# Optimization experiments

Measured on AMD Instinct MI355X. Metric: run time of the kernel, lower is better.

The kernel has to match this reference:

```python
import jax, jax.numpy as jnp
import numpy as np

M, N, K, D_IN = 200, 6, 25, 784
GAMMA, EPS = 0.5, 0.5
TOTAL = M * N


def setup_inputs() -> dict:
    key = jax.random.key(0)
    ks = jax.random.split(key, 8)
    B = 16384
    def lin(kk, shape, fan_in):
        bound = 1.0 / np.sqrt(fan_in)
        return jax.random.uniform(kk, shape, jnp.float32, -bound, bound)
    return {
        "batch_x": jax.random.normal(ks[0], (B, D_IN), jnp.float32),
        "Wa": lin(ks[1], (M, D_IN), D_IN),
        "ba": lin(ks[2], (M,), D_IN),
        "Wb": lin(ks[3], (TOTAL, TOTAL), TOTAL),
        "bb": lin(ks[4], (TOTAL,), TOTAL),
        "Wd": lin(ks[5], (D_IN, M), M),
        "bd": lin(ks[6], (D_IN,), M),
    }


def _step(params, carry, x):
    Wa, ba, Wb, bb, Wd, bd = params
    x_b, phi, psi = carry
    # sigma: per-group drive broadcast over cells + full recurrent term, shape (m, n)
    z_a = (Wa @ x + ba)[:, None]                      # (m, 1)
    z_b = (Wb @ x_b + bb).reshape(M, N)               # (m, n)
    sigma = z_a + z_b
    # inhibited activity
    pi = (1.0 - phi) * (sigma - sigma.min() + 1.0)    # (m, n)
    lambda_i = pi.max(axis=1)                         # (m,)
    # top-1 cell per group (scatter of topk indices == one-hot argmax)
    M_pi = jax.nn.one_hot(jnp.argmax(pi, axis=1), N, dtype=sigma.dtype)
    # top-k groups
    _, idx = jax.lax.top_k(lambda_i, K)
    M_lambda = jnp.zeros((M,), sigma.dtype).at[idx].set(1.0)[:, None]
    y = jnp.tanh(M_pi * M_lambda * sigma)             # (m, n)
    x_a_pred = Wd @ y.max(axis=1) + bd                # (D_in,)
    # memory / inhibition updates
    psi_n = jnp.maximum(EPS * psi, y)
    phi_n = jnp.maximum(GAMMA * phi, y)
    alpha = psi_n.sum()
    alpha = jnp.where(alpha == 0.0, 1.0, alpha)
    x_b_n = (psi_n / alpha).reshape(-1)
    # original detaches the recurrent state each step
    carry_n = (jax.lax.stop_gradient(x_b_n),
               jax.lax.stop_gradient(phi_n),
               jax.lax.stop_gradient(psi_n))
    return carry_n, x_a_pred


def reference(batch_x, Wa, ba, Wb, bb, Wd, bd):
    params = (Wa, ba, Wb, bb, Wd, bd)
    carry0 = (jnp.zeros((TOTAL,), batch_x.dtype),
              jnp.zeros((M, N), batch_x.dtype),
              jnp.zeros((M, N), batch_x.dtype))
    (x_b, phi, psi), preds = jax.lax.scan(
        lambda c, x: _step(params, c, x), carry0, batch_x)
    return preds, x_b, phi, psi
```

## Files before the change

kernel.cpp:

```cpp
#include <hip/hip_runtime.h>
#include <math.h>

#define Tn   16384
#define Mg   200
#define Nc   6
#define TOT  1200
#define Kk   25
#define Din  784
#define CH   32

__global__ void transpose_k(const float* __restrict__ src, float* __restrict__ dst,
                            int R, int C) {
    __shared__ float tile[32][33];
    int bx = blockIdx.x * 32, by = blockIdx.y * 32;
    int x = bx + threadIdx.x;
    for (int j = 0; j < 32; j += 8) {
        int y = by + threadIdx.y + j;
        if (x < C && y < R) tile[threadIdx.y + j][threadIdx.x] = src[(size_t)y * C + x];
    }
    __syncthreads();
    int x2 = by + threadIdx.x;
    for (int j = 0; j < 32; j += 8) {
        int y2 = bx + threadIdx.y + j;
        if (x2 < R && y2 < C) dst[(size_t)y2 * R + x2] = tile[threadIdx.x][threadIdx.y + j];
    }
}

__global__ void za_k(const float* __restrict__ X, const float* __restrict__ Wa,
                     const float* __restrict__ ba, float* __restrict__ Za) {
    __shared__ float xs[16][788];
    const int tid = threadIdx.x;
    const int t0  = blockIdx.x * 16;
    for (int idx = tid; idx < 16 * Din; idx += 256) {
        int tt = idx / Din, kk = idx - tt * Din;
        xs[tt][kk] = X[(size_t)(t0 + tt) * Din + kk];
    }
    __syncthreads();
    const int tq = tid & 15, gq = tid >> 4;
    const float4* xrow = reinterpret_cast<const float4*>(&xs[tq][0]);
    for (int g = gq; g < Mg; g += 16) {
        float acc = ba[g];
        const float4* wrow = reinterpret_cast<const float4*>(Wa + (size_t)g * Din);
        for (int k4 = 0; k4 < Din / 4; ++k4) {
            float4 a = xrow[k4], b = wrow[k4];
            acc = fmaf(a.x, b.x, acc); acc = fmaf(a.y, b.y, acc);
            acc = fmaf(a.z, b.z, acc); acc = fmaf(a.w, b.w, acc);
        }
        Za[(size_t)(t0 + tq) * Mg + g] = acc;
    }
}

__launch_bounds__(256, 1)
__global__ void serial_k(const float* __restrict__ Za, const float* __restrict__ WbT,
                         const float* __restrict__ bb,
                         unsigned long long* __restrict__ YP,
                         float* __restrict__ outTail) {
    __shared__ alignas(16) unsigned long long lamk[Mg];
    __shared__ alignas(16) unsigned long long sel[26];
    __shared__ alignas(16) float red[4];
    __shared__ alignas(16) float zs[CH * Mg];
    __shared__ alignas(16) unsigned long long ypk[CH * Kk];

    const int tid = threadIdx.x;
    const bool own = (tid < Mg);
    const int b = Nc * tid;

    float u0=0.f,u1=0.f,u2=0.f,u3=0.f,u4=0.f,u5=0.f;
    float p0=0.f,p1=0.f,p2=0.f,p3=0.f,p4=0.f,p5=0.f;
    float b0=0.f,b1=0.f,b2=0.f,b3=0.f,b4=0.f,b5=0.f;
    float alpha = 0.f;
    if (own) {
        b0=bb[b]; b1=bb[b+1]; b2=bb[b+2]; b3=bb[b+3]; b4=bb[b+4]; b5=bb[b+5];
    }
    #pragma unroll
    for (int i = 0; i < 7; ++i) {
        int idx = i * 1024 + tid * 4;
        if (idx < CH * Mg) {
            float4 v = *reinterpret_cast<const float4*>(Za + idx);
            *reinterpret_cast<float4*>(zs + idx) = v;
        }
    }
    __syncthreads();

    const float* baseW = WbT + b;

    for (int t = 0; t < Tn; ++t) {
        const int tc = t & (CH - 1);

        float s0=0,s1=0,s2=0,s3=0,s4=0,s5=0;
        float lmin = INFINITY;
        if (own) {
            float zbv = zs[tc * Mg + tid];
            float inv = (alpha == 0.f) ? 1.f : (1.f / alpha);
            s0 = fmaf(u0, inv, b0 + zbv); s1 = fmaf(u1, inv, b1 + zbv);
            s2 = fmaf(u2, inv, b2 + zbv); s3 = fmaf(u3, inv, b3 + zbv);
            s4 = fmaf(u4, inv, b4 + zbv); s5 = fmaf(u5, inv, b5 + zbv);
            lmin = fminf(fminf(fminf(s0,s1),fminf(s2,s3)),fminf(s4,s5));
        }
        for (int o = 32; o; o >>= 1) lmin = fminf(lmin, __shfl_down(lmin, o));
        if ((tid & 63) == 0) red[tid >> 6] = lmin;
        __syncthreads();

        unsigned long long myk = 0ull;
        float sb=0.f, pb=0.f; int bj = 0;
        if (own) {
            float4 r4 = *reinterpret_cast<const float4*>(red);
            float m1 = 1.f - fminf(fminf(r4.x, r4.y), fminf(r4.z, r4.w));
            float best = -INFINITY;
            float sa[6] = {s0,s1,s2,s3,s4,s5};
            float pa[6] = {p0,p1,p2,p3,p4,p5};
            #pragma unroll
            for (int j = 0; j < Nc; ++j) {
                float pv = (1.f - pa[j]) * (sa[j] + m1);
                if (pv > best) { best = pv; bj = j; sb = sa[j]; pb = pa[j]; }
            }
            unsigned ub = __float_as_uint(best);
            ub ^= (unsigned)(((int)ub) >> 31) | 0x80000000u;
            myk = ((unsigned long long)ub << 32) | (unsigned long long)(0xFFFFFFFFu - (unsigned)tid);
            lamk[tid] = myk;
        }
        __syncthreads();

        if (own) {
            float y  = tanhf(sb);
            float yv = fmaxf(y, 0.f);
            float dc = fmaxf(y - 0.5f * pb, 0.f);
            int r = 0;
            const ulonglong2* L = reinterpret_cast<const ulonglong2*>(lamk);
            #pragma unroll
            for (int qq = 0; qq < Mg / 2; ++qq) {
                ulonglong2 kv = L[qq];
                r += (kv.x > myk) + (kv.y > myk);
            }
            float d = 0.f;
            if (r < Kk) {
                d = dc;
                sel[r] = ((unsigned long long)(unsigned)((b + bj) * TOT) << 32) |
                         (unsigned long long)__float_as_uint(d);
                ypk[tc * Kk + r] = ((unsigned long long)(unsigned)tid << 32) |
                                   (unsigned long long)__float_as_uint(yv);
            }
            p0 = 0.5f*p0 + ((bj==0)?d:0.f); p1 = 0.5f*p1 + ((bj==1)?d:0.f);
            p2 = 0.5f*p2 + ((bj==2)?d:0.f); p3 = 0.5f*p3 + ((bj==3)?d:0.f);
            p4 = 0.5f*p4 + ((bj==4)?d:0.f); p5 = 0.5f*p5 + ((bj==5)?d:0.f);
        }
        __syncthreads();

        if (own) {
            ulonglong2 sraw[13];
            const ulonglong2* S = reinterpret_cast<const ulonglong2*>(sel);
            #pragma unroll
            for (int qq = 0; qq < 13; ++qq) sraw[qq] = S[qq];
            float sd[Kk]; int so[Kk];
            #pragma unroll
            for (int k = 0; k < Kk; ++k) {
                unsigned long long v = (k & 1) ? sraw[k >> 1].y : sraw[k >> 1].x;
                sd[k] = __uint_as_float((unsigned)v);
                so[k] = (int)(v >> 32);
            }
            float asum = 0.f;
            #pragma unroll
            for (int k = 0; k < Kk; ++k) asum += sd[k];
            alpha = 0.5f * alpha + asum;

            float2 c0[Kk], c1[Kk], c2[Kk];
            #pragma unroll
            for (int k = 0; k < Kk; ++k) {
                const float* cp = baseW + so[k];
                c0[k] = *reinterpret_cast<const float2*>(cp);
                c1[k] = *reinterpret_cast<const float2*>(cp + 2);
                c2[k] = *reinterpret_cast<const float2*>(cp + 4);
            }
            __builtin_amdgcn_sched_barrier(0);
            float a0=0.5f*u0, a1=0.5f*u1, a2=0.5f*u2, a3=0.5f*u3, a4=0.5f*u4, a5=0.5f*u5;
            #pragma unroll
            for (int k = 0; k < Kk; ++k) {
                float dk = sd[k];
                a0 = fmaf(dk, c0[k].x, a0); a1 = fmaf(dk, c0[k].y, a1);
                a2 = fmaf(dk, c1[k].x, a2); a3 = fmaf(dk, c1[k].y, a3);
                a4 = fmaf(dk, c2[k].x, a4); a5 = fmaf(dk, c2[k].y, a5);
            }
            u0=a0; u1=a1; u2=a2; u3=a3; u4=a4; u5=a5;
        }

        if (tc == CH - 1) {
            const size_t t0 = (size_t)(t - (CH - 1)) * Kk;
            for (int i = tid; i < CH * Kk; i += 256)
                YP[t0 + i] = ypk[i];
            if (t + 1 < Tn) {
                const float* src = Za + (size_t)(t + 1) * Mg;
                #pragma unroll
                for (int i = 0; i < 7; ++i) {
                    int idx = i * 1024 + tid * 4;
                    if (idx < CH * Mg) {
                        float4 v = *reinterpret_cast<const float4*>(src + idx);
                        *reinterpret_cast<float4*>(zs + idx) = v;
                    }
                }
            }
            __syncthreads();
        }
    }

    if (own) {
        float inv = (alpha == 0.f) ? 1.f : (1.f / alpha);
        float pa[6] = {p0,p1,p2,p3,p4,p5};
        #pragma unroll
        for (int j = 0; j < Nc; ++j) {
            outTail[b + j]           = pa[j] * inv;
            outTail[TOT + b + j]     = pa[j];
            outTail[2 * TOT + b + j] = pa[j];
        }
    }
}

__global__ void preds_k(const unsigned long long* __restrict__ YP,
                        const float* __restrict__ WdT, const float* __restrict__ bd,
                        float* __restrict__ out) {
    const int t = blockIdx.x;
    __shared__ float sv[Kk];
    __shared__ int   si[Kk];
    if (threadIdx.x < Kk) {
        unsigned long long v = YP[(size_t)t * Kk + threadIdx.x];
        sv[threadIdx.x] = __uint_as_float((unsigned)v);
        si[threadIdx.x] = (int)(v >> 32);
    }
    __syncthreads();
    for (int d = threadIdx.x; d < Din; d += 256) {
        float acc = bd[d];
        #pragma unroll
        for (int k = 0; k < Kk; ++k)
            acc = fmaf(sv[k], WdT[(size_t)si[k] * Din + d], acc);
        out[(size_t)t * Din + d] = acc;
    }
}

extern "C" void kernel_launch(void* const* d_in, const int* in_sizes, int n_in,
                              void* d_out, int out_size, void* d_ws, size_t ws_size,
                              hipStream_t stream) {
    const float* X  = (const float*)d_in[0];
    const float* Wa = (const float*)d_in[1];
    const float* ba = (const float*)d_in[2];
    const float* Wb = (const float*)d_in[3];
    const float* bb = (const float*)d_in[4];
    const float* Wd = (const float*)d_in[5];
    const float* bd = (const float*)d_in[6];
    float* out = (float*)d_out;

    float* w    = (float*)d_ws;
    float* Za   = w;
    float* WbT  = Za  + (size_t)Tn * Mg;
    float* WdT  = WbT + (size_t)TOT * TOT;
    unsigned long long* YP =
        (unsigned long long*)(WdT + (size_t)Mg * Din);

    dim3 tb(32, 8);
    transpose_k<<<dim3((TOT + 31) / 32, (TOT + 31) / 32), tb, 0, stream>>>(Wb, WbT, TOT, TOT);
    transpose_k<<<dim3((Mg + 31) / 32, (Din + 31) / 32), tb, 0, stream>>>(Wd, WdT, Din, Mg);
    za_k<<<Tn / 16, 256, 0, stream>>>(X, Wa, ba, Za);
    serial_k<<<1, 256, 0, stream>>>(Za, WbT, bb, YP, out + (size_t)Tn * Din);
    preds_k<<<Tn, 256, 0, stream>>>(YP, WdT, bd, out);
}
```

Baseline: 78.09 ms.

## Run serial recurrence in a single wavefront with ballot-based top-k selection

The serial kernel shrinks from 256 threads to a single 64-lane wavefront, with each lane owning four groups (24 cells). Block-wide __syncthreads barriers and the O(M) rank-counting top-k are replaced by wave shuffles for the min and a ballot/popcount quickselect for the 25th-largest key. It also swaps tanhf for an exp/rcp approximation and double-buffers the float4 weight-row loads. In exchange, each lane does four times the per-step work and holds much more register state, and the quickselect loop has a data-dependent iteration count.

```diff
diff --git a/kernel.cpp b/kernel.cpp
--- a/kernel.cpp
+++ b/kernel.cpp
@@ -50,166 +50,235 @@
     }
 }
 
-__launch_bounds__(256, 1)
+__launch_bounds__(64, 1)
 __global__ void serial_k(const float* __restrict__ Za, const float* __restrict__ WbT,
                          const float* __restrict__ bb,
                          unsigned long long* __restrict__ YP,
                          float* __restrict__ outTail) {
-    __shared__ alignas(16) unsigned long long lamk[Mg];
-    __shared__ alignas(16) unsigned long long sel[26];
-    __shared__ alignas(16) float red[4];
     __shared__ alignas(16) float zs[CH * Mg];
     __shared__ alignas(16) unsigned long long ypk[CH * Kk];
-
-    const int tid = threadIdx.x;
-    const bool own = (tid < Mg);
-    const int b = Nc * tid;
-
-    float u0=0.f,u1=0.f,u2=0.f,u3=0.f,u4=0.f,u5=0.f;
-    float p0=0.f,p1=0.f,p2=0.f,p3=0.f,p4=0.f,p5=0.f;
-    float b0=0.f,b1=0.f,b2=0.f,b3=0.f,b4=0.f,b5=0.f;
+    __shared__ alignas(16) unsigned long long selL[26];
+
+    const int lane = threadIdx.x;
+    const bool grp = (lane < 50);
+    const int cell0 = 24 * lane;
+
+    float u[24], ps[24], cb[24];
+    #pragma unroll
+    for (int i = 0; i < 24; ++i) { u[i] = 0.f; ps[i] = 0.f; cb[i] = 0.f; }
+    if (grp) {
+        #pragma unroll
+        for (int i = 0; i < 6; ++i) {
+            float4 v = *reinterpret_cast<const float4*>(bb + cell0 + 4 * i);
+            cb[4*i] = v.x; cb[4*i+1] = v.y; cb[4*i+2] = v.z; cb[4*i+3] = v.w;
+        }
+    }
+    if (lane == 0) selL[25] = 0ull;
     float alpha = 0.f;
-    if (own) {
-        b0=bb[b]; b1=bb[b+1]; b2=bb[b+2]; b3=bb[b+3]; b4=bb[b+4]; b5=bb[b+5];
-    }
+
     #pragma unroll
-    for (int i = 0; i < 7; ++i) {
-        int idx = i * 1024 + tid * 4;
-        if (idx < CH * Mg) {
-            float4 v = *reinterpret_cast<const float4*>(Za + idx);
-            *reinterpret_cast<float4*>(zs + idx) = v;
-        }
-    }
-    __syncthreads();
-
-    const float* baseW = WbT + b;
+    for (int j = 0; j < 25; ++j) {
+        int f = lane + j * 64;
+        *reinterpret_cast<float4*>(zs + 4 * f) =
+            *reinterpret_cast<const float4*>(Za + 4 * f);
+    }
+
+    const unsigned long long lt = (1ull << lane) - 1ull;
 
     for (int t = 0; t < Tn; ++t) {
         const int tc = t & (CH - 1);
 
-        float s0=0,s1=0,s2=0,s3=0,s4=0,s5=0;
-        float lmin = INFINITY;
-        if (own) {
-            float zbv = zs[tc * Mg + tid];
-            float inv = (alpha == 0.f) ? 1.f : (1.f / alpha);
-            s0 = fmaf(u0, inv, b0 + zbv); s1 = fmaf(u1, inv, b1 + zbv);
-            s2 = fmaf(u2, inv, b2 + zbv); s3 = fmaf(u3, inv, b3 + zbv);
-            s4 = fmaf(u4, inv, b4 + zbv); s5 = fmaf(u5, inv, b5 + zbv);
-            lmin = fminf(fminf(fminf(s0,s1),fminf(s2,s3)),fminf(s4,s5));
-        }
-        for (int o = 32; o; o >>= 1) lmin = fminf(lmin, __shfl_down(lmin, o));
-        if ((tid & 63) == 0) red[tid >> 6] = lmin;
-        __syncthreads();
-
-        unsigned long long myk = 0ull;
-        float sb=0.f, pb=0.f; int bj = 0;
-        if (own) {
-            float4 r4 = *reinterpret_cast<const float4*>(red);
-            float m1 = 1.f - fminf(fminf(r4.x, r4.y), fminf(r4.z, r4.w));
-            float best = -INFINITY;
-            float sa[6] = {s0,s1,s2,s3,s4,s5};
-            float pa[6] = {p0,p1,p2,p3,p4,p5};
-            #pragma unroll
-            for (int j = 0; j < Nc; ++j) {
-                float pv = (1.f - pa[j]) * (sa[j] + m1);
-                if (pv > best) { best = pv; bj = j; sb = sa[j]; pb = pa[j]; }
-            }
-            unsigned ub = __float_as_uint(best);
-            ub ^= (unsigned)(((int)ub) >> 31) | 0x80000000u;
-            myk = ((unsigned long long)ub << 32) | (unsigned long long)(0xFFFFFFFFu - (unsigned)tid);
-            lamk[tid] = myk;
-        }
-        __syncthreads();
-
-        if (own) {
-            float y  = tanhf(sb);
-            float yv = fmaxf(y, 0.f);
-            float dc = fmaxf(y - 0.5f * pb, 0.f);
-            int r = 0;
-            const ulonglong2* L = reinterpret_cast<const ulonglong2*>(lamk);
-            #pragma unroll
-            for (int qq = 0; qq < Mg / 2; ++qq) {
-                ulonglong2 kv = L[qq];
-                r += (kv.x > myk) + (kv.y > myk);
-            }
+        float4 za4 = make_float4(0.f, 0.f, 0.f, 0.f);
+        if (grp) za4 = *reinterpret_cast<const float4*>(zs + tc * Mg + 4 * lane);
+
+        const float A0  = (alpha == 0.f) ? 1.f : alpha;
+        const float inv = 1.f / A0;
+
+        float sg[24];
+        float lm = INFINITY;
+        if (grp) {
+            #pragma unroll
+            for (int c = 0; c < 4; ++c) {
+                float zc = (c == 0) ? za4.x : (c == 1) ? za4.y : (c == 2) ? za4.z : za4.w;
+                #pragma unroll
+                for (int j = 0; j < 6; ++j) {
+                    int i = 6 * c + j;
+                    sg[i] = fmaf(u[i], inv, cb[i] + zc);
+                    lm = fminf(lm, sg[i]);
+                }
+            }
+        }
+        #pragma unroll
+        for (int o = 1; o < 64; o <<= 1) lm = fminf(lm, __shfl_xor(lm, o));
+        const float m1 = 1.f - lm;
+
+        float bs[4], bp[4]; int bj[4]; unsigned long long kb[4];
+        #pragma unroll
+        for (int c = 0; c < 4; ++c) { bs[c] = 0.f; bp[c] = 0.f; bj[c] = 0; kb[c] = 0ull; }
+        if (grp) {
+            #pragma unroll
+            for (int c = 0; c < 4; ++c) {
+                float best = -INFINITY, sbv = 0.f, pbv = 0.f; int jb = 0;
+                #pragma unroll
+                for (int j = 0; j < 6; ++j) {
+                    int i = 6 * c + j;
+                    float pv = (1.f - ps[i]) * (sg[i] + m1);
+                    bool bet = pv > best;
+                    best = bet ? pv : best;
+                    jb  = bet ? j : jb;
+                    sbv = bet ? sg[i] : sbv;
+                    pbv = bet ? ps[i] : pbv;
+                }
+                unsigned ub = __float_as_uint(best);
+                ub ^= (unsigned)(((int)ub) >> 31) | 0x80000000u;
+                int g = 4 * lane + c;
+                kb[c] = ((unsigned long long)ub << 32) |
+                        (unsigned long long)(0xFFFFFFFFu - (unsigned)g);
+                bs[c] = sbv; bp[c] = pbv; bj[c] = jb;
+            }
+        }
+
+        unsigned long long A = 0ull, B = ~0ull;
+        unsigned long long p = __shfl(kb[0], 0);
+        unsigned long long theta;
+        while (true) {
+            int cnt = __popcll(__ballot(kb[0] >= p)) + __popcll(__ballot(kb[1] >= p))
+                    + __popcll(__ballot(kb[2] >= p)) + __popcll(__ballot(kb[3] >= p));
+            if (cnt == Kk) { theta = p; break; }
+            if (cnt > Kk) A = p; else B = p;
+            unsigned long long m0 = __ballot(kb[0] > A && kb[0] < B);
+            unsigned long long m1b = __ballot(kb[1] > A && kb[1] < B);
+            unsigned long long m2 = __ballot(kb[2] > A && kb[2] < B);
+            unsigned long long m3 = __ballot(kb[3] > A && kb[3] < B);
+            int cls; unsigned long long mm;
+            if (m0)       { cls = 0; mm = m0; }
+            else if (m1b) { cls = 1; mm = m1b; }
+            else if (m2)  { cls = 2; mm = m2; }
+            else          { cls = 3; mm = m3; }
+            int sl = __ffsll(mm) - 1;
+            unsigned long long kc = (cls == 0) ? kb[0] : (cls == 1) ? kb[1]
+                                  : (cls == 2) ? kb[2] : kb[3];
+            p = __shfl(kc, sl);
+        }
+
+        unsigned long long M0 = __ballot(kb[0] >= theta);
+        unsigned long long M1 = __ballot(kb[1] >= theta);
+        unsigned long long M2 = __ballot(kb[2] >= theta);
+        unsigned long long M3 = __ballot(kb[3] >= theta);
+        int base0 = 0;
+        int base1 = __popcll(M0);
+        int base2 = base1 + __popcll(M1);
+        int base3 = base2 + __popcll(M2);
+
+        #pragma unroll
+        for (int c = 0; c < 4; ++c) {
+            unsigned long long Mc = (c == 0) ? M0 : (c == 1) ? M1 : (c == 2) ? M2 : M3;
+            int bsee = (c == 0) ? base0 : (c == 1) ? base1 : (c == 2) ? base2 : base3;
+            bool s = grp && (kb[c] >= theta);
             float d = 0.f;
-            if (r < Kk) {
-                d = dc;
-                sel[r] = ((unsigned long long)(unsigned)((b + bj) * TOT) << 32) |
-                         (unsigned long long)__float_as_uint(d);
-                ypk[tc * Kk + r] = ((unsigned long long)(unsigned)tid << 32) |
-                                   (unsigned long long)__float_as_uint(yv);
-            }
-            p0 = 0.5f*p0 + ((bj==0)?d:0.f); p1 = 0.5f*p1 + ((bj==1)?d:0.f);
-            p2 = 0.5f*p2 + ((bj==2)?d:0.f); p3 = 0.5f*p3 + ((bj==3)?d:0.f);
-            p4 = 0.5f*p4 + ((bj==4)?d:0.f); p5 = 0.5f*p5 + ((bj==5)?d:0.f);
-        }
-        __syncthreads();
-
-        if (own) {
-            ulonglong2 sraw[13];
-            const ulonglong2* S = reinterpret_cast<const ulonglong2*>(sel);
-            #pragma unroll
-            for (int qq = 0; qq < 13; ++qq) sraw[qq] = S[qq];
-            float sd[Kk]; int so[Kk];
-            #pragma unroll
-            for (int k = 0; k < Kk; ++k) {
-                unsigned long long v = (k & 1) ? sraw[k >> 1].y : sraw[k >> 1].x;
-                sd[k] = __uint_as_float((unsigned)v);
-                so[k] = (int)(v >> 32);
-            }
-            float asum = 0.f;
-            #pragma unroll
-            for (int k = 0; k < Kk; ++k) asum += sd[k];
-            alpha = 0.5f * alpha + asum;
-
-            float2 c0[Kk], c1[Kk], c2[Kk];
-            #pragma unroll
-            for (int k = 0; k < Kk; ++k) {
-                const float* cp = baseW + so[k];
-                c0[k] = *reinterpret_cast<const float2*>(cp);
-                c1[k] = *reinterpret_cast<const float2*>(cp + 2);
-                c2[k] = *reinterpret_cast<const float2*>(cp + 4);
-            }
-            __builtin_amdgcn_sched_barrier(0);
-            float a0=0.5f*u0, a1=0.5f*u1, a2=0.5f*u2, a3=0.5f*u3, a4=0.5f*u4, a5=0.5f*u5;
-            #pragma unroll
-            for (int k = 0; k < Kk; ++k) {
-                float dk = sd[k];
-                a0 = fmaf(dk, c0[k].x, a0); a1 = fmaf(dk, c0[k].y, a1);
-                a2 = fmaf(dk, c1[k].x, a2); a3 = fmaf(dk, c1[k].y, a3);
-                a4 = fmaf(dk, c2[k].x, a4); a5 = fmaf(dk, c2[k].y, a5);
-            }
-            u0=a0; u1=a1; u2=a2; u3=a3; u4=a4; u5=a5;
+            if (s) {
+                int slot = bsee + __popcll(Mc & lt);
+                float x = fminf(fmaxf(bs[c], -9.f), 9.f);
+                float e = __expf(2.f * x);
+                float y = (e - 1.f) * __builtin_amdgcn_rcpf(e + 1.f);
+                float yv = fmaxf(y, 0.f);
+                d = fmaxf(y - 0.5f * bp[c], 0.f);
+                int g = 4 * lane + c;
+                ypk[tc * Kk + slot] = ((unsigned long long)(unsigned)g << 32) |
+                                      (unsigned long long)__float_as_uint(yv);
+                int eix = 6 * g + bj[c];
+                selL[slot] = ((unsigned long long)(unsigned)eix << 32) |
+                             (unsigned long long)__float_as_uint(d);
+            }
+            #pragma unroll
+            for (int j = 0; j < 6; ++j) {
+                int i = 6 * c + j;
+                float add = (j == bj[c]) ? d : 0.f;
+                ps[i] = fmaf(ps[i], 0.5f, add);
+            }
+        }
+
+        ulonglong2 sr[13];
+        #pragma unroll
+        for (int q = 0; q < 13; ++q)
+            sr[q] = reinterpret_cast<const ulonglong2*>(selL)[q];
+        float sd[Kk]; int se[Kk];
+        #pragma unroll
+        for (int k = 0; k < Kk; ++k) {
+            unsigned long long v = (k & 1) ? sr[k >> 1].y : sr[k >> 1].x;
+            sd[k] = __uint_as_float((unsigned)v);
+            se[k] = (int)(v >> 32);
+        }
+        float asum = 0.f;
+        #pragma unroll
+        for (int k = 0; k < Kk; ++k) asum += sd[k];
+        alpha = fmaf(alpha, 0.5f, asum);
+
+        #pragma unroll
+        for (int i = 0; i < 24; ++i) u[i] *= 0.5f;
+        if (grp) {
+            const float* wp = WbT + cell0;
+            float4 buf[2][5][6];
+            #pragma unroll
+            for (int k = 0; k < 5; ++k) {
+                const float* cp = wp + (size_t)se[k] * TOT;
+                #pragma unroll
+                for (int q = 0; q < 6; ++q)
+                    buf[0][k][q] = *reinterpret_cast<const float4*>(cp + 4 * q);
+            }
+            #pragma unroll
+            for (int b = 0; b < 5; ++b) {
+                if (b < 4) {
+                    #pragma unroll
+                    for (int k = 0; k < 5; ++k) {
+                        const float* cp = wp + (size_t)se[5 * (b + 1) + k] * TOT;
+                        #pragma unroll
+                        for (int q = 0; q < 6; ++q)
+                            buf[(b + 1) & 1][k][q] =
+                                *reinterpret_cast<const float4*>(cp + 4 * q);
+                    }
+                }
+                #pragma unroll
+                for (int k = 0; k < 5; ++k) {
+                    float dk = sd[5 * b + k];
+                    #pragma unroll
+                    for (int q = 0; q < 6; ++q) {
+                        float4 w = buf[b & 1][k][q];
+                        u[4*q+0] = fmaf(dk, w.x, u[4*q+0]);
+                        u[4*q+1] = fmaf(dk, w.y, u[4*q+1]);
+                        u[4*q+2] = fmaf(dk, w.z, u[4*q+2]);
+                        u[4*q+3] = fmaf(dk, w.w, u[4*q+3]);
+                    }
+                }
+            }
         }
 
         if (tc == CH - 1) {
             const size_t t0 = (size_t)(t - (CH - 1)) * Kk;
-            for (int i = tid; i < CH * Kk; i += 256)
-                YP[t0 + i] = ypk[i];
+            #pragma unroll
+            for (int j = 0; j < 13; ++j) {
+                int i = lane + j * 64;
+                if (i < CH * Kk) YP[t0 + i] = ypk[i];
+            }
             if (t + 1 < Tn) {
                 const float* src = Za + (size_t)(t + 1) * Mg;
                 #pragma unroll
-                for (int i = 0; i < 7; ++i) {
-                    int idx = i * 1024 + tid * 4;
-                    if (idx < CH * Mg) {
-                        float4 v = *reinterpret_cast<const float4*>(src + idx);
-                        *reinterpret_cast<float4*>(zs + idx) = v;
-                    }
-                }
-            }
-            __syncthreads();
-        }
-    }
-
-    if (own) {
-        float inv = (alpha == 0.f) ? 1.f : (1.f / alpha);
-        float pa[6] = {p0,p1,p2,p3,p4,p5};
-        #pragma unroll
-        for (int j = 0; j < Nc; ++j) {
-            outTail[b + j]           = pa[j] * inv;
-            outTail[TOT + b + j]     = pa[j];
-            outTail[2 * TOT + b + j] = pa[j];
+                for (int j = 0; j < 25; ++j) {
+                    int f = lane + j * 64;
+                    *reinterpret_cast<float4*>(zs + 4 * f) =
+                        *reinterpret_cast<const float4*>(src + 4 * f);
+                }
+            }
+        }
+    }
+
+    if (grp) {
+        float inv2 = (alpha == 0.f) ? 1.f : (1.f / alpha);
+        #pragma unroll
+        for (int i = 0; i < 24; ++i) {
+            outTail[cell0 + i]           = ps[i] * inv2;
+            outTail[TOT + cell0 + i]     = ps[i];
+            outTail[2 * TOT + cell0 + i] = ps[i];
         }
     }
 }
@@ -258,6 +327,6 @@
     transpose_k<<<dim3((TOT + 31) / 32, (TOT + 31) / 32), tb, 0, stream>>>(Wb, WbT, TOT, TOT);
     transpose_k<<<dim3((Mg + 31) / 32, (Din + 31) / 32), tb, 0, stream>>>(Wd, WdT, Din, Mg);
     za_k<<<Tn / 16, 256, 0, stream>>>(X, Wa, ba, Za);
-    serial_k<<<1, 256, 0, stream>>>(Za, WbT, bb, YP, out + (size_t)Tn * Din);
+    serial_k<<<1, 64, 0, stream>>>(Za, WbT, bb, YP, out + (size_t)Tn * Din);
     preds_k<<<Tn, 256, 0, stream>>>(YP, WdT, bd, out);
 }
```

After: 104.4 ms. +33.7%, slower.
